# Kernel tuning notes

Hardware: AMD Instinct MI355X
Metric: run time of the kernel (lower is better)

Reference implementation:

```python
import jax, jax.numpy as jnp
import numpy as np

BLOCK = 16
H = 16
KV = 4
HPG = H // KV
DH = 64
SCALE = 1.0 / np.sqrt(DH).astype(np.float32)


def setup_inputs() -> dict:
    key = jax.random.key(0)
    ks = jax.random.split(key, 7)
    B, Ldec, Lenc, D = 2, 8192, 4096, 1024
    s = 1.0 / np.sqrt(D).astype(np.float32)
    return {
        "hidden_states": jax.random.normal(ks[0], (B, Ldec, D), jnp.float32),
        "encoder_hidden_states": jax.random.normal(ks[1], (B, Lenc, D), jnp.float32),
        "attention_mask": jax.random.randint(ks[2], (B, Lenc), 0, 2, jnp.int32),
        "Wq": jax.random.normal(ks[3], (D, H * DH), jnp.float32) * s,
        "Wk": jax.random.normal(ks[4], (D, KV * DH), jnp.float32) * s,
        "Wv": jax.random.normal(ks[5], (D, KV * DH), jnp.float32) * s,
        "Wo": jax.random.normal(ks[6], (H * DH, D), jnp.float32) * s,
    }


def reference(hidden_states, encoder_hidden_states, attention_mask, Wq, Wk, Wv, Wo):
    B, Ldec, D = hidden_states.shape
    Lenc = encoder_hidden_states.shape[1]
    pad = (BLOCK - Ldec % BLOCK) % BLOCK
    x = jnp.pad(hidden_states, ((0, 0), (0, pad), (0, 0))) if pad else hidden_states
    nb = (Ldec + pad) // BLOCK
    # mean-pool decoder tokens into blocks: [B, nb, D]
    pooled = x.reshape(B, nb, BLOCK, D).mean(axis=2)
    # projections; GQA: group q heads by kv head (repeat_interleave order)
    q = (pooled @ Wq).reshape(B, nb, KV, HPG, DH)          # [B, nb, KV, HPG, DH]
    k = (encoder_hidden_states @ Wk).reshape(B, Lenc, KV, DH)
    v = (encoder_hidden_states @ Wv).reshape(B, Lenc, KV, DH)
    scores = jnp.einsum("bngqd,blgd->bgqnl", q, k) * SCALE  # [B, KV, HPG, nb, Lenc]
    mask = (attention_mask == 0)[:, None, None, None, :]
    scores = jnp.where(mask, jnp.float32(-1e9), scores)
    attn = jax.nn.softmax(scores, axis=-1)
    out = jnp.einsum("bgqnl,blgd->bngqd", attn, v)          # [B, nb, KV, HPG, DH]
    out = out.reshape(B, nb, H * DH) @ Wo                   # [B, nb, D]
    # broadcast block output back to token level
    unpooled = jnp.broadcast_to(out[:, :, None, :], (B, nb, BLOCK, D)).reshape(B, nb * BLOCK, D)
    return unpooled[:, :Ldec, :]
```

## Files before the change

kernel.cpp:

```cpp
#include <hip/hip_runtime.h>


typedef unsigned short u16;
typedef __attribute__((ext_vector_type(8))) __bf16 bf16x8;
typedef __attribute__((ext_vector_type(4))) float f32x4;
typedef __attribute__((ext_vector_type(4))) _Float16 f16x4;

static __device__ __forceinline__ u16 f2bf(float f) {
    unsigned int u = __float_as_uint(f);
    u = (u + 0x7fffu + ((u >> 16) & 1u)) >> 16;
    return (u16)u;
}
static __device__ __forceinline__ void gload16(const u16* g, u16* l) {
    __builtin_amdgcn_global_load_lds(
        (const __attribute__((address_space(1))) void*)g,
        (__attribute__((address_space(3))) void*)l, 16, 0, 0);
}

__global__ __launch_bounds__(256) void prep_all(const float* __restrict__ enc,
                                                const float* __restrict__ hid,
                                                const int* __restrict__ mask,
                                                const float* __restrict__ Wq,
                                                const float* __restrict__ Wk,
                                                const float* __restrict__ Wv,
                                                const float* __restrict__ Wo,
                                                u16* __restrict__ encb,
                                                u16* __restrict__ poolb,
                                                u16* __restrict__ mh,
                                                u16* __restrict__ Wq_t,
                                                u16* __restrict__ Wkv_t,
                                                u16* __restrict__ Wo_t) {
    int bid = blockIdx.x;
    if (bid < 2560) {
        const float* in; u16* out; int N, nbx, rowoff;
        if (bid < 1024)      { in = Wq; out = Wq_t;  N = 1024; nbx = 32; rowoff = 0; }
        else if (bid < 2048) { in = Wo; out = Wo_t;  N = 1024; nbx = 32; rowoff = 0; bid -= 1024; }
        else if (bid < 2304) { in = Wk; out = Wkv_t; N = 256;  nbx = 8;  rowoff = 0; bid -= 2048; }
        else                 { in = Wv; out = Wkv_t; N = 256;  nbx = 8;  rowoff = 256; bid -= 2304; }
        const int n0 = (bid % nbx) * 32, k0 = (bid / nbx) * 32;
        __shared__ float t[32][33];
        const int tx = threadIdx.x & 31, ty = threadIdx.x >> 5;
#pragma unroll
        for (int i = 0; i < 4; ++i)
            t[ty + 8 * i][tx] = in[(size_t)(k0 + ty + 8 * i) * N + n0 + tx];
        __syncthreads();
#pragma unroll
        for (int i = 0; i < 4; ++i)
            out[(size_t)(rowoff + n0 + ty + 8 * i) * 1024 + k0 + tx] = f2bf(t[tx][ty + 8 * i]);
    } else if (bid < 4608) {
        const int base = (bid - 2560) * 1024 + threadIdx.x;
        float4 v[4];
#pragma unroll
        for (int j = 0; j < 4; ++j) v[j] = ((const float4*)enc)[base + j * 256];
#pragma unroll
        for (int j = 0; j < 4; ++j) {
            ushort4 o;
            o.x = f2bf(v[j].x); o.y = f2bf(v[j].y);
            o.z = f2bf(v[j].z); o.w = f2bf(v[j].w);
            ((ushort4*)encb)[base + j * 256] = o;
        }
    } else if (bid < 5632) {
        const int tid = (bid - 4608) * 256 + threadIdx.x;
        const int c4 = tid & 255;
        const int row = tid >> 8;
        const float4* src = (const float4*)(hid + (size_t)row * 16 * 1024) + c4;
        float4 a = src[0];
#pragma unroll
        for (int t = 1; t < 16; ++t) {
            float4 b = src[(size_t)t * 256];
            a.x += b.x; a.y += b.y; a.z += b.z; a.w += b.w;
        }
        ushort4 o;
        o.x = f2bf(a.x * 0.0625f); o.y = f2bf(a.y * 0.0625f);
        o.z = f2bf(a.z * 0.0625f); o.w = f2bf(a.w * 0.0625f);
        *(ushort4*)(poolb + (size_t)row * 1024 + c4 * 4) = o;
    } else {
#pragma unroll
        for (int k = 0; k < 32; ++k) {
            const int i = threadIdx.x + 256 * k;
            mh[i] = mask[i] ? (u16)0x3C00 : (u16)0;
        }
    }
}

template <int MODE>
static __device__ __forceinline__ void gemm_core(const u16* __restrict__ A,
                                                 const u16* __restrict__ Bt,
                                                 const int* __restrict__ maskp,
                                                 u16* __restrict__ outK,
                                                 u16* __restrict__ outV,
                                                 float* __restrict__ out_f,
                                                 int m0, int n0, int kt0, int nkt) {
    __shared__ __align__(16) u16 sAB[2 * 64 * 72];
    u16* sA = sAB;
    u16* sB = sAB + 64 * 64;
    const int t = threadIdx.x;
    const int w = t >> 6, lane = t & 63, quad = lane >> 4, r16 = lane & 15;
    const int row8 = lane >> 3, seg = lane & 7;

    f32x4 acc[4];
#pragma unroll
    for (int i = 0; i < 4; ++i) acc[i] = (f32x4){0.f, 0.f, 0.f, 0.f};

    for (int kt = kt0; kt < kt0 + nkt; ++kt) {
        const int k0 = kt * 64;
        __syncthreads();
#pragma unroll
        for (int j = 0; j < 2; ++j) {
            const int ra = w * 16 + j * 8;
            gload16(A + (size_t)(m0 + ra + row8) * 1024 + k0 + seg * 8, sA + ra * 64);
            gload16(Bt + (size_t)(n0 + ra + row8) * 1024 + k0 + seg * 8, sB + ra * 64);
        }
        __syncthreads();
#pragma unroll
        for (int kk = 0; kk < 2; ++kk) {
            const bf16x8 af = *(const bf16x8*)(sA + (16 * w + r16) * 64 + kk * 32 + quad * 8);
#pragma unroll
            for (int nt = 0; nt < 4; ++nt) {
                const bf16x8 bfv = *(const bf16x8*)(sB + (nt * 16 + r16) * 64 + kk * 32 + quad * 8);
                acc[nt] = __builtin_amdgcn_mfma_f32_16x16x32_bf16(af, bfv, acc[nt], 0, 0, 0);
            }
        }
    }

    if (MODE == 0) {
#pragma unroll
        for (int nt = 0; nt < 4; ++nt)
#pragma unroll
            for (int r = 0; r < 4; ++r) {
                const int m = m0 + 16 * w + quad * 4 + r;
                const int c = n0 + nt * 16 + r16;
                const int b = m >> 9, nq = m & 511, g = c >> 8, qh = (c >> 6) & 3, d = c & 63;
                outK[((((size_t)(b * 4 + g) * 4 + qh) * 512 + nq) << 6) + d] =
                    f2bf(acc[nt][r] * 0.180336880f);
            }
    } else if (MODE == 4) {
        const bool isV = (n0 >= 256);
        const int g = (isV ? (n0 - 256) : n0) >> 6;
        const int b = m0 >> 12, l0 = m0 & 4095;
        u16* sT = sAB;
        __syncthreads();
        if (isV) {
            float mfl[4];
#pragma unroll
            for (int r = 0; r < 4; ++r)
                mfl[r] = maskp[b * 4096 + l0 + 16 * w + quad * 4 + r] ? 1.f : 0.f;
#pragma unroll
            for (int nt = 0; nt < 4; ++nt)
#pragma unroll
                for (int r = 0; r < 4; ++r) {
                    const int ml = 16 * w + quad * 4 + r, cl = nt * 16 + r16;
                    union { _Float16 h; u16 u; } cv;
                    cv.h = (_Float16)(acc[nt][r] * mfl[r]);
                    sT[cl * 72 + ml] = cv.u;
                }
        } else {
#pragma unroll
            for (int nt = 0; nt < 4; ++nt)
#pragma unroll
                for (int r = 0; r < 4; ++r) {
                    const int ml = 16 * w + quad * 4 + r, cl = nt * 16 + r16;
                    sT[ml * 72 + cl] = f2bf(acc[nt][r]);
                }
        }
        __syncthreads();
#pragma unroll
        for (int p = 0; p < 2; ++p) {
            const int idx = t + 256 * p, rr = idx >> 3, ch = idx & 7;
            const int4 v = *(const int4*)(sT + rr * 72 + ch * 8);
            if (isV)
                *(int4*)(outV + ((size_t)(b * 4 + g) * 64 + rr) * 4096 + l0 + ch * 8) = v;
            else
                *(int4*)(outK + (((size_t)(b * 4 + g) * 4096 + l0 + rr) << 6) + ch * 8) = v;
        }
    } else {
#pragma unroll
        for (int nt = 0; nt < 4; ++nt)
#pragma unroll
            for (int r = 0; r < 4; ++r) {
                const int m = m0 + 16 * w + quad * 4 + r;
                const int c = n0 + nt * 16 + r16;
                out_f[(size_t)m * 1024 + c] = acc[nt][r];
            }
    }
}

__global__ __launch_bounds__(256) void gemm_qkv(const u16* __restrict__ poolb,
                                                const u16* __restrict__ encb,
                                                const u16* __restrict__ Wq_t,
                                                const u16* __restrict__ Wkv_t,
                                                const int* __restrict__ maskp,
                                                u16* __restrict__ Qa,
                                                u16* __restrict__ Ka,
                                                u16* __restrict__ Va) {
    const int bx = blockIdx.x;
    if (bx < 1024) {
        gemm_core<4>(encb, Wkv_t, maskp, Ka, Va, nullptr, (bx >> 3) * 64, (bx & 7) * 64, 0, 16);
    } else {
        const int b = bx - 1024;
        gemm_core<0>(poolb, Wq_t, nullptr, Qa, nullptr, nullptr, (b >> 4) * 64, (b & 15) * 64, 0, 16);
    }
}

__global__ __launch_bounds__(256) void gemm_o(const u16* __restrict__ attn,
                                              const u16* __restrict__ Wo_t,
                                              float* __restrict__ blkpart) {
    const int bx = blockIdx.x;
    const int s = bx >> 8, m0 = ((bx >> 4) & 15) * 64, n0 = (bx & 15) * 64;
    gemm_core<3>(attn, Wo_t, nullptr, nullptr, nullptr,
                 blkpart + ((size_t)s << 20), m0, n0, s * 4, 4);
}

__global__ __launch_bounds__(256, 4) void flash_attn(const u16* __restrict__ Qa,
                                                     const u16* __restrict__ Ka,
                                                     const u16* __restrict__ Vt,
                                                     const u16* __restrict__ mh,
                                                     float* __restrict__ Opart,
                                                     float* __restrict__ mlpart) {
    const int bx = blockIdx.x;
    const int s16 = bx & 31, rr = bx >> 5;
    const int split = rr & 3, gb = rr >> 2;
    const int g = gb & 3, b = gb >> 2;
    __shared__ __align__(16) u16 sK[64 * 72];
    __shared__ __align__(16) u16 sV[64 * 68];
    const int t = threadIdx.x;
    const int qh = t >> 6, lane = t & 63, quad = lane >> 4, r16 = lane & 15;

    bf16x8 aq[2];
    {
        const size_t qbase = ((((size_t)(b * 4 + g) * 4 + qh) * 512) + s16 * 16 + r16) * 64;
#pragma unroll
        for (int kk = 0; kk < 2; ++kk)
            aq[kk] = *(const bf16x8*)(Qa + qbase + kk * 32 + quad * 8);
    }
    const u16* Kg = Ka + (size_t)(b * 4 + g) * 4096 * 64 + (size_t)split * 1024 * 64;
    const u16* Vg = Vt + (size_t)(b * 4 + g) * 64 * 4096 + split * 1024;
    const u16* mb = mh + b * 4096 + split * 1024 + quad * 4;

    f32x4 o[4], lacc;
#pragma unroll
    for (int i = 0; i < 4; ++i) o[i] = (f32x4){0.f, 0.f, 0.f, 0.f};
    lacc = (f32x4){0.f, 0.f, 0.f, 0.f};

    for (int tile = 0; tile < 16; ++tile) {
        const int l0 = tile * 64;
        __syncthreads();
#pragma unroll
        for (int p = 0; p < 2; ++p) {
            const int idx = t + 256 * p, row = idx >> 3, seg = idx & 7;
            *(int4*)(sK + row * 72 + seg * 8) =
                *(const int4*)(Kg + (size_t)(l0 + row) * 64 + seg * 8);
            *(int4*)(sV + row * 68 + seg * 8) =
                *(const int4*)(Vg + (size_t)row * 4096 + l0 + seg * 8);
        }
        __syncthreads();

        f32x4 st[4];
#pragma unroll
        for (int nt = 0; nt < 4; ++nt) st[nt] = (f32x4){0.f, 0.f, 0.f, 0.f};
#pragma unroll
        for (int kk = 0; kk < 2; ++kk)
#pragma unroll
            for (int nt = 0; nt < 4; ++nt) {
                const bf16x8 ka = *(const bf16x8*)(sK + (nt * 16 + r16) * 72 + kk * 32 + quad * 8);
                st[nt] = __builtin_amdgcn_mfma_f32_16x16x32_bf16(ka, aq[kk], st[nt], 0, 0, 0);
            }

#pragma unroll
        for (int nt = 0; nt < 4; ++nt) {
            f16x4 pa;
#pragma unroll
            for (int j = 0; j < 4; ++j)
                pa[j] = (_Float16)__builtin_amdgcn_exp2f(st[nt][j]);
            const f16x4 bvm = *(const f16x4*)(mb + l0 + nt * 16);
            lacc = __builtin_amdgcn_mfma_f32_16x16x16f16(pa, bvm, lacc, 0, 0, 0);
#pragma unroll
            for (int dt = 0; dt < 4; ++dt) {
                const f16x4 bv = *(const f16x4*)(sV + (dt * 16 + r16) * 68 + nt * 16 + quad * 4);
                o[dt] = __builtin_amdgcn_mfma_f32_16x16x16f16(pa, bv, o[dt], 0, 0, 0);
            }
        }
    }

    const size_t pbase = ((size_t)bx * 4 + qh) * 1024;
#pragma unroll
    for (int dt = 0; dt < 4; ++dt)
#pragma unroll
        for (int r = 0; r < 4; ++r)
            Opart[pbase + (size_t)(quad * 4 + r) * 64 + dt * 16 + r16] = o[dt][r];
    if (r16 == 0) {
#pragma unroll
        for (int r = 0; r < 4; ++r)
            mlpart[((size_t)bx * 4 + qh) * 16 + quad * 4 + r] = lacc[r];
    }
}

__global__ __launch_bounds__(256) void flash_combine(const float* __restrict__ Opart,
                                                     const float* __restrict__ mlpart,
                                                     u16* __restrict__ attnout) {
    const int bx = blockIdx.x;
    const int s16 = bx & 31, h = bx >> 5;
    const int qh = h & 3, g = (h >> 2) & 3, b = h >> 4;
    const int t = threadIdx.x;
    const int q = t >> 4, dg = t & 15;
    float4 a = make_float4(0.f, 0.f, 0.f, 0.f);
    float L = 0.f;
#pragma unroll
    for (int s = 0; s < 4; ++s) {
        const size_t part = (((size_t)((b * 4 + g) * 4 + s) * 32 + s16) * 4 + qh);
        const float4 v = *(const float4*)(Opart + part * 1024 + q * 64 + dg * 4);
        a.x += v.x; a.y += v.y; a.z += v.z; a.w += v.w;
        L += mlpart[part * 16 + q];
    }
    const float invL = 1.f / L;
    ushort4 ov;
    ov.x = f2bf(a.x * invL); ov.y = f2bf(a.y * invL);
    ov.z = f2bf(a.z * invL); ov.w = f2bf(a.w * invL);
    *(ushort4*)(attnout + ((size_t)b * 512 + s16 * 16 + q) * 1024 +
                (g * 4 + qh) * 64 + dg * 4) = ov;
}

__global__ __launch_bounds__(256) void bcast_out(const float* __restrict__ blkpart,
                                                 float* __restrict__ out) {
    const int tid = blockIdx.x * 256 + threadIdx.x;
    const int c4 = tid & 255;
    const int row = tid >> 8;
    float4 a = make_float4(0.f, 0.f, 0.f, 0.f);
#pragma unroll
    for (int s = 0; s < 4; ++s) {
        const float4 v = ((const float4*)blkpart)[(s << 18) + (row << 8) + c4];
        a.x += v.x; a.y += v.y; a.z += v.z; a.w += v.w;
    }
    const int b = row >> 9, n = row & 511;
    float4* dst = (float4*)out + (((size_t)b * 8192 + n * 16) << 8) + c4;
#pragma unroll
    for (int rep = 0; rep < 16; ++rep)
        dst[(size_t)rep << 8] = a;
}

extern "C" void kernel_launch(void* const* d_in, const int* in_sizes, int n_in,
                              void* d_out, int out_size, void* d_ws, size_t ws_size,
                              hipStream_t stream) {
    const float* hid  = (const float*)d_in[0];
    const float* enc  = (const float*)d_in[1];
    const int*   mask = (const int*)d_in[2];
    const float* Wq   = (const float*)d_in[3];
    const float* Wk   = (const float*)d_in[4];
    const float* Wv   = (const float*)d_in[5];
    const float* Wo   = (const float*)d_in[6];
    float* out = (float*)d_out;

    char* ws = (char*)d_ws;
    size_t off = 0;
    auto alloc = [&](size_t bytes) -> char* {
        char* p = ws + off;
        off += (bytes + 255) & ~(size_t)255;
        return p;
    };
    u16* Wq_t  = (u16*)alloc((size_t)1024 * 1024 * 2);
    u16* Wkv_t = (u16*)alloc((size_t)512 * 1024 * 2);
    u16* Wo_t  = (u16*)alloc((size_t)1024 * 1024 * 2);
    u16* encb  = (u16*)alloc((size_t)8192 * 1024 * 2);
    u16* poolb = (u16*)alloc((size_t)1024 * 1024 * 2);
    u16* Qa    = (u16*)alloc((size_t)1024 * 1024 * 2);
    u16* Ka    = (u16*)alloc((size_t)8 * 4096 * 64 * 2);
    u16* Va    = (u16*)alloc((size_t)8 * 4096 * 64 * 2);
    u16* attn  = (u16*)alloc((size_t)1024 * 1024 * 2);
    u16* mh    = (u16*)alloc((size_t)8192 * 2);
    float* Opart   = (float*)encb;
    float* blkpart = (float*)encb;
    float* mlpart  = (float*)poolb;

    prep_all<<<5633, 256, 0, stream>>>(enc, hid, mask, Wq, Wk, Wv, Wo,
                                       encb, poolb, mh, Wq_t, Wkv_t, Wo_t);
    gemm_qkv<<<1280, 256, 0, stream>>>(poolb, encb, Wq_t, Wkv_t, mask, Qa, Ka, Va);
    flash_attn<<<1024, 256, 0, stream>>>(Qa, Ka, Va, mh, Opart, mlpart);
    flash_combine<<<1024, 256, 0, stream>>>(Opart, mlpart, attn);
    gemm_o<<<1024, 256, 0, stream>>>(attn, Wo_t, blkpart);
    bcast_out<<<1024, 256, 0, stream>>>(blkpart, out);
}
```

Baseline: 248.5 us.

## Use 128x64 tiles for K/V projection GEMM and reorder prep blocks

The K/V projection GEMM moves from 64x64 to 128x64 output tiles, so each wave computes two 16-row slabs and reuses the loaded B fragment across them. This halves the number of K/V blocks (1024 to 512) and cuts redundant weight-tile loads. Shared memory is now passed into gemm_core from the caller and grows to 24 KB in gemm_qkv. The prep kernel also reorders its block ranges so pooling and encoder conversion are scheduled before the weight transposes. The larger tile raises register and LDS use per block, which may lower occupancy.

Result: no change. 243.6 us (-2.0%).

```diff
diff --git a/kernel.cpp b/kernel.cpp
--- a/kernel.cpp
+++ b/kernel.cpp
@@ -31,7 +31,35 @@
                                                 u16* __restrict__ Wkv_t,
                                                 u16* __restrict__ Wo_t) {
     int bid = blockIdx.x;
-    if (bid < 2560) {
+    if (bid < 1024) {
+        const int tid = bid * 256 + threadIdx.x;
+        const int c4 = tid & 255;
+        const int row = tid >> 8;
+        const float4* src = (const float4*)(hid + (size_t)row * 16 * 1024) + c4;
+        float4 a = src[0];
+#pragma unroll
+        for (int t = 1; t < 16; ++t) {
+            float4 b = src[(size_t)t * 256];
+            a.x += b.x; a.y += b.y; a.z += b.z; a.w += b.w;
+        }
+        ushort4 o;
+        o.x = f2bf(a.x * 0.0625f); o.y = f2bf(a.y * 0.0625f);
+        o.z = f2bf(a.z * 0.0625f); o.w = f2bf(a.w * 0.0625f);
+        *(ushort4*)(poolb + (size_t)row * 1024 + c4 * 4) = o;
+    } else if (bid < 3072) {
+        const int base = (bid - 1024) * 1024 + threadIdx.x;
+        float4 v[4];
+#pragma unroll
+        for (int j = 0; j < 4; ++j) v[j] = ((const float4*)enc)[base + j * 256];
+#pragma unroll
+        for (int j = 0; j < 4; ++j) {
+            ushort4 o;
+            o.x = f2bf(v[j].x); o.y = f2bf(v[j].y);
+            o.z = f2bf(v[j].z); o.w = f2bf(v[j].w);
+            ((ushort4*)encb)[base + j * 256] = o;
+        }
+    } else if (bid < 5632) {
+        bid -= 3072;
         const float* in; u16* out; int N, nbx, rowoff;
         if (bid < 1024)      { in = Wq; out = Wq_t;  N = 1024; nbx = 32; rowoff = 0; }
         else if (bid < 2048) { in = Wo; out = Wo_t;  N = 1024; nbx = 32; rowoff = 0; bid -= 1024; }
@@ -47,33 +75,6 @@
 #pragma unroll
         for (int i = 0; i < 4; ++i)
             out[(size_t)(rowoff + n0 + ty + 8 * i) * 1024 + k0 + tx] = f2bf(t[tx][ty + 8 * i]);
-    } else if (bid < 4608) {
-        const int base = (bid - 2560) * 1024 + threadIdx.x;
-        float4 v[4];
-#pragma unroll
-        for (int j = 0; j < 4; ++j) v[j] = ((const float4*)enc)[base + j * 256];
-#pragma unroll
-        for (int j = 0; j < 4; ++j) {
-            ushort4 o;
-            o.x = f2bf(v[j].x); o.y = f2bf(v[j].y);
-            o.z = f2bf(v[j].z); o.w = f2bf(v[j].w);
-            ((ushort4*)encb)[base + j * 256] = o;
-        }
-    } else if (bid < 5632) {
-        const int tid = (bid - 4608) * 256 + threadIdx.x;
-        const int c4 = tid & 255;
-        const int row = tid >> 8;
-        const float4* src = (const float4*)(hid + (size_t)row * 16 * 1024) + c4;
-        float4 a = src[0];
-#pragma unroll
-        for (int t = 1; t < 16; ++t) {
-            float4 b = src[(size_t)t * 256];
-            a.x += b.x; a.y += b.y; a.z += b.z; a.w += b.w;
-        }
-        ushort4 o;
-        o.x = f2bf(a.x * 0.0625f); o.y = f2bf(a.y * 0.0625f);
-        o.z = f2bf(a.z * 0.0625f); o.w = f2bf(a.w * 0.0625f);
-        *(ushort4*)(poolb + (size_t)row * 1024 + c4 * 4) = o;
     } else {
 #pragma unroll
         for (int k = 0; k < 32; ++k) {
@@ -86,12 +87,10 @@
 template <int MODE>
 static __device__ __forceinline__ void gemm_core(const u16* __restrict__ A,
                                                  const u16* __restrict__ Bt,
-                                                 const int* __restrict__ maskp,
-                                                 u16* __restrict__ outK,
-                                                 u16* __restrict__ outV,
+                                                 u16* __restrict__ outQ,
                                                  float* __restrict__ out_f,
-                                                 int m0, int n0, int kt0, int nkt) {
-    __shared__ __align__(16) u16 sAB[2 * 64 * 72];
+                                                 int m0, int n0, int kt0, int nkt,
+                                                 u16* sAB) {
     u16* sA = sAB;
     u16* sB = sAB + 64 * 64;
     const int t = threadIdx.x;
@@ -131,48 +130,9 @@
                 const int m = m0 + 16 * w + quad * 4 + r;
                 const int c = n0 + nt * 16 + r16;
                 const int b = m >> 9, nq = m & 511, g = c >> 8, qh = (c >> 6) & 3, d = c & 63;
-                outK[((((size_t)(b * 4 + g) * 4 + qh) * 512 + nq) << 6) + d] =
+                outQ[((((size_t)(b * 4 + g) * 4 + qh) * 512 + nq) << 6) + d] =
                     f2bf(acc[nt][r] * 0.180336880f);
             }
-    } else if (MODE == 4) {
-        const bool isV = (n0 >= 256);
-        const int g = (isV ? (n0 - 256) : n0) >> 6;
-        const int b = m0 >> 12, l0 = m0 & 4095;
-        u16* sT = sAB;
-        __syncthreads();
-        if (isV) {
-            float mfl[4];
-#pragma unroll
-            for (int r = 0; r < 4; ++r)
-                mfl[r] = maskp[b * 4096 + l0 + 16 * w + quad * 4 + r] ? 1.f : 0.f;
-#pragma unroll
-            for (int nt = 0; nt < 4; ++nt)
-#pragma unroll
-                for (int r = 0; r < 4; ++r) {
-                    const int ml = 16 * w + quad * 4 + r, cl = nt * 16 + r16;
-                    union { _Float16 h; u16 u; } cv;
-                    cv.h = (_Float16)(acc[nt][r] * mfl[r]);
-                    sT[cl * 72 + ml] = cv.u;
-                }
-        } else {
-#pragma unroll
-            for (int nt = 0; nt < 4; ++nt)
-#pragma unroll
-                for (int r = 0; r < 4; ++r) {
-                    const int ml = 16 * w + quad * 4 + r, cl = nt * 16 + r16;
-                    sT[ml * 72 + cl] = f2bf(acc[nt][r]);
-                }
-        }
-        __syncthreads();
-#pragma unroll
-        for (int p = 0; p < 2; ++p) {
-            const int idx = t + 256 * p, rr = idx >> 3, ch = idx & 7;
-            const int4 v = *(const int4*)(sT + rr * 72 + ch * 8);
-            if (isV)
-                *(int4*)(outV + ((size_t)(b * 4 + g) * 64 + rr) * 4096 + l0 + ch * 8) = v;
-            else
-                *(int4*)(outK + (((size_t)(b * 4 + g) * 4096 + l0 + rr) << 6) + ch * 8) = v;
-        }
     } else {
 #pragma unroll
         for (int nt = 0; nt < 4; ++nt)
@@ -193,22 +153,110 @@
                                                 u16* __restrict__ Qa,
                                                 u16* __restrict__ Ka,
                                                 u16* __restrict__ Va) {
+    __shared__ __align__(16) u16 smem[12288];
     const int bx = blockIdx.x;
-    if (bx < 1024) {
-        gemm_core<4>(encb, Wkv_t, maskp, Ka, Va, nullptr, (bx >> 3) * 64, (bx & 7) * 64, 0, 16);
+    if (bx >= 512) {
+        const int b = bx - 512;
+        gemm_core<0>(poolb, Wq_t, Qa, nullptr, (b >> 4) * 64, (b & 15) * 64, 0, 16, smem);
+        return;
+    }
+    const int m0 = (bx >> 3) * 128, n0 = (bx & 7) * 64;
+    u16* sA = smem;
+    u16* sB = smem + 128 * 64;
+    const int t = threadIdx.x;
+    const int w = t >> 6, lane = t & 63, quad = lane >> 4, r16 = lane & 15;
+    const int row8 = lane >> 3, seg = lane & 7;
+
+    f32x4 acc[2][4];
+#pragma unroll
+    for (int i = 0; i < 2; ++i)
+#pragma unroll
+        for (int nt = 0; nt < 4; ++nt) acc[i][nt] = (f32x4){0.f, 0.f, 0.f, 0.f};
+
+    for (int kt = 0; kt < 16; ++kt) {
+        const int k0 = kt * 64;
+        __syncthreads();
+#pragma unroll
+        for (int p = 0; p < 4; ++p) {
+            const int ra = p * 32 + w * 8;
+            gload16(encb + (size_t)(m0 + ra + row8) * 1024 + k0 + seg * 8, sA + ra * 64);
+        }
+#pragma unroll
+        for (int p = 0; p < 2; ++p) {
+            const int ra = p * 32 + w * 8;
+            gload16(Wkv_t + (size_t)(n0 + ra + row8) * 1024 + k0 + seg * 8, sB + ra * 64);
+        }
+        __syncthreads();
+#pragma unroll
+        for (int kk = 0; kk < 2; ++kk)
+#pragma unroll
+            for (int i = 0; i < 2; ++i) {
+                const bf16x8 af = *(const bf16x8*)(sA + (w * 32 + i * 16 + r16) * 64 + kk * 32 + quad * 8);
+#pragma unroll
+                for (int nt = 0; nt < 4; ++nt) {
+                    const bf16x8 bfv = *(const bf16x8*)(sB + (nt * 16 + r16) * 64 + kk * 32 + quad * 8);
+                    acc[i][nt] = __builtin_amdgcn_mfma_f32_16x16x32_bf16(af, bfv, acc[i][nt], 0, 0, 0);
+                }
+            }
+    }
+
+    const bool isV = (n0 >= 256);
+    const int g = (isV ? (n0 - 256) : n0) >> 6;
+    const int b = m0 >> 12, l0 = m0 & 4095;
+    __syncthreads();
+    if (isV) {
+        u16* sT = smem;
+#pragma unroll
+        for (int i = 0; i < 2; ++i) {
+            float mfl[4];
+#pragma unroll
+            for (int r = 0; r < 4; ++r)
+                mfl[r] = maskp[b * 4096 + l0 + w * 32 + i * 16 + quad * 4 + r] ? 1.f : 0.f;
+#pragma unroll
+            for (int nt = 0; nt < 4; ++nt)
+#pragma unroll
+                for (int r = 0; r < 4; ++r) {
+                    const int ml = w * 32 + i * 16 + quad * 4 + r, cl = nt * 16 + r16;
+                    union { _Float16 h; u16 u; } cv;
+                    cv.h = (_Float16)(acc[i][nt][r] * mfl[r]);
+                    sT[cl * 136 + ml] = cv.u;
+                }
+        }
+        __syncthreads();
+#pragma unroll
+        for (int p = 0; p < 4; ++p) {
+            const int idx = t + 256 * p, rr = idx >> 4, ch = idx & 15;
+            *(int4*)(Va + ((size_t)(b * 4 + g) * 64 + rr) * 4096 + l0 + ch * 8) =
+                *(const int4*)(sT + rr * 136 + ch * 8);
+        }
     } else {
-        const int b = bx - 1024;
-        gemm_core<0>(poolb, Wq_t, nullptr, Qa, nullptr, nullptr, (b >> 4) * 64, (b & 15) * 64, 0, 16);
+        u16* sT = smem;
+#pragma unroll
+        for (int i = 0; i < 2; ++i)
+#pragma unroll
+            for (int nt = 0; nt < 4; ++nt)
+#pragma unroll
+                for (int r = 0; r < 4; ++r) {
+                    const int ml = w * 32 + i * 16 + quad * 4 + r, cl = nt * 16 + r16;
+                    sT[ml * 72 + cl] = f2bf(acc[i][nt][r]);
+                }
+        __syncthreads();
+#pragma unroll
+        for (int p = 0; p < 4; ++p) {
+            const int idx = t + 256 * p, rr = idx >> 3, ch = idx & 7;
+            *(int4*)(Ka + (((size_t)(b * 4 + g) * 4096 + l0 + rr) << 6) + ch * 8) =
+                *(const int4*)(sT + rr * 72 + ch * 8);
+        }
     }
 }
 
 __global__ __launch_bounds__(256) void gemm_o(const u16* __restrict__ attn,
                                               const u16* __restrict__ Wo_t,
                                               float* __restrict__ blkpart) {
+    __shared__ __align__(16) u16 smem[8192];
     const int bx = blockIdx.x;
     const int s = bx >> 8, m0 = ((bx >> 4) & 15) * 64, n0 = (bx & 15) * 64;
-    gemm_core<3>(attn, Wo_t, nullptr, nullptr, nullptr,
-                 blkpart + ((size_t)s << 20), m0, n0, s * 4, 4);
+    gemm_core<3>(attn, Wo_t, nullptr, blkpart + ((size_t)s << 20), m0, n0, s * 4, 4, smem);
 }
 
 __global__ __launch_bounds__(256, 4) void flash_attn(const u16* __restrict__ Qa,
@@ -373,7 +421,7 @@
 
     prep_all<<<5633, 256, 0, stream>>>(enc, hid, mask, Wq, Wk, Wv, Wo,
                                        encb, poolb, mh, Wq_t, Wkv_t, Wo_t);
-    gemm_qkv<<<1280, 256, 0, stream>>>(poolb, encb, Wq_t, Wkv_t, mask, Qa, Ka, Va);
+    gemm_qkv<<<768, 256, 0, stream>>>(poolb, encb, Wq_t, Wkv_t, mask, Qa, Ka, Va);
     flash_attn<<<1024, 256, 0, stream>>>(Qa, Ka, Va, mh, Opart, mlpart);
     flash_combine<<<1024, 256, 0, stream>>>(Opart, mlpart, attn);
     gemm_o<<<1024, 256, 0, stream>>>(attn, Wo_t, blkpart);
```
